# Performance work log

Hardware: AMD Instinct MI355X
Metric: run time of the kernel (lower is better)

Reference implementation:

```python
import jax, jax.numpy as jnp
import numpy as np

B, F, T, K = 16, 256, 2048, 20
TEMP = 0.5
EPS = 1e-8  # torch cosine_similarity eps


def setup_inputs() -> dict:
    key = jax.random.key(0)
    k1, k2, k3 = jax.random.split(key, 3)
    z = jax.random.normal(k1, (B, F, T), dtype=jnp.float32)
    c = jax.random.normal(k2, (B, F, T + 1), dtype=jnp.float32)
    # torch: torch.randint(0, full_len - 1, size=(B, T * K))  -> values in [0, T-2]
    negative_inds = jax.random.randint(k3, (B, T * K), 0, T - 1, dtype=jnp.int64)
    return {"z": z, "c": c, "negative_inds": negative_inds}


def reference(z, c, negative_inds):
    # ---- _generate_negatives ----
    # z: [B, F, T] -> flat rows [B*T, F]
    z_flat = jnp.transpose(z, (0, 2, 1)).reshape(-1, F)
    # per-batch offset i*T (torch adds it in-place for i in 1..B-1)
    inds = negative_inds + (jnp.arange(B, dtype=negative_inds.dtype) * T)[:, None]
    negatives = z_flat[inds.reshape(-1)].reshape(B, T, K, F)

    # ---- _calculate_similarity ----
    c_t = jnp.transpose(c[..., 1:], (0, 2, 1))[:, :, None, :]  # [B, T, 1, F] (drop start token)
    z_t = jnp.transpose(z, (0, 2, 1))[:, :, None, :]           # [B, T, 1, F]
    neg_is_pos = jnp.all(c_t == negatives, axis=-1)            # [B, T, K]
    targets = jnp.concatenate([c_t, negatives], axis=-2)       # [B, T, K+1, F]

    num = jnp.sum(z_t * targets, axis=-1)                      # [B, T, K+1]
    denom = jnp.maximum(
        jnp.linalg.norm(z_t, axis=-1) * jnp.linalg.norm(targets, axis=-1), EPS
    )
    logits = (num / denom) / TEMP                              # [B, T, K+1]

    # mask negatives that exactly equal the positive (wav2vec2-style)
    pad = jnp.zeros_like(neg_is_pos[..., :1])
    full_mask = jnp.concatenate([pad, neg_is_pos], axis=-1)    # [B, T, K+1]
    logits = jnp.where(full_mask, -jnp.inf, logits)

    return logits.reshape(-1, K + 1)                           # [B*T, K+1]
```

## Files before the change

### kernel.cpp

```cpp
#include <hip/hip_runtime.h>
#include <hip/hip_fp16.h>
#include <math.h>

#define B_ 16
#define F_ 256
#define T_ 2048
#define K_ 20
#define OUTK 21
#define NPAIR 10

typedef float v2f __attribute__((ext_vector_type(2)));

#if __has_builtin(__builtin_amdgcn_cvt_pk_f32_fp8) && __has_builtin(__builtin_amdgcn_cvt_pk_fp8_f32)
#define HW_FP8 1
#else
#define HW_FP8 0
#endif

#if !HW_FP8
__device__ __forceinline__ float dec_fp8(unsigned v) {
    unsigned s = (v >> 7) & 1, e = (v >> 3) & 15, m = v & 7;
    float r = e ? __uint_as_float(((e + 120u) << 23) | (m << 20))
                : (float)m * 0.001953125f;
    return s ? -r : r;
}
__device__ __forceinline__ unsigned enc_fp8(float x) {
    unsigned bits = __float_as_uint(x);
    unsigned s = bits >> 31;
    unsigned a = bits & 0x7fffffffu;
    float ax = __uint_as_float(a);
    unsigned r;
    if (ax < 0.015625f) {
        r = (unsigned)(int)(ax * 512.f + 0.5f);
    } else {
        int e = (int)(a >> 23) - 127;
        unsigned m = a & 0x7fffffu;
        unsigned keep = m >> 20, rest = m & 0xFFFFFu;
        keep += (rest > 0x80000u) || (rest == 0x80000u && (keep & 1));
        if (keep == 8) { keep = 0; ++e; }
        r = ((unsigned)(e + 7) << 3) | keep;
    }
    return (s << 7) | r;
}
#endif

__device__ __forceinline__ unsigned pack_fp8x4(float a0, float a1, float a2, float a3) {
#if HW_FP8
    int u = 0;
    u = __builtin_amdgcn_cvt_pk_fp8_f32(a0, a1, u, false);
    u = __builtin_amdgcn_cvt_pk_fp8_f32(a2, a3, u, true);
    return (unsigned)u;
#else
    return enc_fp8(a0) | (enc_fp8(a1) << 8) | (enc_fp8(a2) << 16) | (enc_fp8(a3) << 24);
#endif
}
template <bool HI>
__device__ __forceinline__ v2f unpk_fp8(unsigned u) {
#if HW_FP8
    return __builtin_amdgcn_cvt_pk_f32_fp8((int)u, HI);
#else
    v2f r; unsigned x = HI ? (u >> 16) : u;
    r[0] = dec_fp8(x & 0xFF); r[1] = dec_fp8((x >> 8) & 0xFF);
    return r;
#endif
}

__global__ __launch_bounds__(256) void prep_kernel(
    const float* __restrict__ z, const float* __restrict__ c,
    unsigned char* __restrict__ zf8, unsigned char* __restrict__ cf8)
{
    __shared__ float tile[256][33];
    __shared__ float ps[32][9];
    __shared__ float sc[32];
    int which = blockIdx.z;
    const float* src = which ? c : z;
    unsigned char* dst = which ? cf8 : zf8;
    int Lsrc = which ? (T_ + 1) : T_;
    int co   = which;

    int b  = blockIdx.y;
    int t0 = blockIdx.x * 32;
    const float* srcb = src + (size_t)b * F_ * Lsrc;
    int tl = threadIdx.x & 31;
    int fl = threadIdx.x >> 5;
#pragma unroll
    for (int i = 0; i < 32; ++i) {
        int f = i * 8 + fl;
        tile[f][tl] = srcb[(size_t)f * Lsrc + (t0 + tl + co)];
    }
    __syncthreads();
    {
        int col = threadIdx.x & 31, oct = threadIdx.x >> 5;
        float s = 0.f;
#pragma unroll 8
        for (int q = 0; q < 32; ++q) {
            float v = tile[oct * 32 + q][col];
            s = fmaf(v, v, s);
        }
        ps[col][oct] = s;
    }
    __syncthreads();
    if (threadIdx.x < 32) {
        float s = 0.f;
#pragma unroll
        for (int o = 0; o < 8; ++o) s += ps[threadIdx.x][o];
        float n = sqrtf(s);
        sc[threadIdx.x] = (n > 0.f) ? (1.0f / n) : 0.f;
    }
    __syncthreads();
    {
        int j = threadIdx.x & 63, r4 = threadIdx.x >> 6;
#pragma unroll
        for (int it = 0; it < 8; ++it) {
            int row = it * 4 + r4;
            float s = sc[row];
            unsigned u = pack_fp8x4(tile[2 * j][row] * s, tile[2 * j + 1][row] * s,
                                    tile[2 * j + 128][row] * s, tile[2 * j + 129][row] * s);
            ((unsigned*)(dst + ((size_t)b * T_ + t0 + row) * F_))[j] = u;
        }
    }
}

__device__ __forceinline__ float dpp_half_sum(float x) {
    x += __int_as_float(__builtin_amdgcn_mov_dpp(__float_as_int(x), 0x111, 0xF, 0xF, true));
    x += __int_as_float(__builtin_amdgcn_mov_dpp(__float_as_int(x), 0x112, 0xF, 0xF, true));
    x += __int_as_float(__builtin_amdgcn_mov_dpp(__float_as_int(x), 0x114, 0xF, 0xF, true));
    x += __int_as_float(__builtin_amdgcn_mov_dpp(__float_as_int(x), 0x118, 0xF, 0xF, true));
    x += __int_as_float(__builtin_amdgcn_mov_dpp(__float_as_int(x), 0x142, 0xF, 0xF, true));
    return x;
}

__global__ __launch_bounds__(256, 8) void sim_kernel(
    const unsigned char* __restrict__ zf8, const unsigned char* __restrict__ cf8,
    const int* __restrict__ inds, float* __restrict__ out)
{
    __shared__ float sd[128];
    int i = blockIdx.x;
    int b = (i & 7) | ((i >= 4096) ? 8 : 0);
    int wid = threadIdx.x >> 6;
    int t = (((i >> 3) & 511) << 2) + wid;
    int lane = threadIdx.x & 63;
    int hl = lane & 31;
    int hi = lane >> 5;
    int bt = __builtin_amdgcn_readfirstlane((b << 11) + t);

    const int* myinds = inds + bt * K_;
    int idxv = myinds[(lane < K_) ? lane : 0];

    uint2 zv8 = ((const uint2*)(zf8 + (size_t)bt * F_))[hl];
    uint2 cv8 = ((const uint2*)(cf8 + (size_t)bt * F_))[hl];

    const char* tbl8 = (const char*)zf8;
    unsigned zbase8  = (unsigned)(b << 11) * 256u;
    unsigned laneoff = (unsigned)hl * 8u;

    uint2 tv[NPAIR];
#pragma unroll
    for (int p = 0; p < NPAIR; ++p) {
        unsigned ilo = (unsigned)__builtin_amdgcn_readlane(idxv, 2 * p);
        unsigned ihi = (unsigned)__builtin_amdgcn_readlane(idxv, 2 * p + 1);
        unsigned off = zbase8 + (hi ? ihi : ilo) * 256u + laneoff;
        tv[p] = *(const uint2*)(tbl8 + off);
    }

    __builtin_amdgcn_sched_barrier(0);

    float zf[8];
    {
        v2f a01 = unpk_fp8<false>(zv8.x), a23 = unpk_fp8<true>(zv8.x);
        v2f a45 = unpk_fp8<false>(zv8.y), a67 = unpk_fp8<true>(zv8.y);
        zf[0] = a01[0]; zf[1] = a01[1]; zf[2] = a23[0]; zf[3] = a23[1];
        zf[4] = a45[0]; zf[5] = a45[1]; zf[6] = a67[0]; zf[7] = a67[1];
    }

    float dc;
    {
        v2f c01 = unpk_fp8<false>(cv8.x), c23 = unpk_fp8<true>(cv8.x);
        v2f c45 = unpk_fp8<false>(cv8.y), c67 = unpk_fp8<true>(cv8.y);
        float d = zf[0] * c01[0];
        d = fmaf(zf[1], c01[1], d);
        d = fmaf(zf[2], c23[0], d);
        d = fmaf(zf[3], c23[1], d);
        d = fmaf(zf[4], c45[0], d);
        d = fmaf(zf[5], c45[1], d);
        d = fmaf(zf[6], c67[0], d);
        d = fmaf(zf[7], c67[1], d);
        dc = d;
    }

    float dz[NPAIR];
#pragma unroll
    for (int p = 0; p < NPAIR; ++p) {
        v2f t01 = unpk_fp8<false>(tv[p].x), t23 = unpk_fp8<true>(tv[p].x);
        v2f t45 = unpk_fp8<false>(tv[p].y), t67 = unpk_fp8<true>(tv[p].y);
        float d = zf[0] * t01[0];
        d = fmaf(zf[1], t01[1], d);
        d = fmaf(zf[2], t23[0], d);
        d = fmaf(zf[3], t23[1], d);
        d = fmaf(zf[4], t45[0], d);
        d = fmaf(zf[5], t45[1], d);
        d = fmaf(zf[6], t67[0], d);
        d = fmaf(zf[7], t67[1], d);
        dz[p] = d;
    }

    unsigned mb = 0;
#pragma unroll
    for (int p = 0; p < NPAIR; ++p) {
        unsigned long long ball = __ballot(tv[p].x == cv8.x);
        unsigned blo = (unsigned)ball, bhi = (unsigned)(ball >> 32);
        if (blo == 0xFFFFFFFFu || bhi == 0xFFFFFFFFu) {
            bool full = (tv[p].x == cv8.x) && (tv[p].y == cv8.y);
            unsigned long long b2 = __ballot(full);
            if ((unsigned)b2 == 0xFFFFFFFFu)          mb |= 1u << (1 + 2 * p);
            if ((unsigned)(b2 >> 32) == 0xFFFFFFFFu)  mb |= 1u << (2 + 2 * p);
        }
    }

    dc = dpp_half_sum(dc);
#pragma unroll
    for (int p = 0; p < NPAIR; ++p) dz[p] = dpp_half_sum(dz[p]);

    if (hl == 31) {
        if (hi == 0) sd[wid * 32] = dc;
#pragma unroll
        for (int p = 0; p < NPAIR; ++p) sd[wid * 32 + 1 + 2 * p + hi] = dz[p];
    }

    if (lane < OUTK) {
        float v = sd[wid * 32 + lane] * 2.0f;
        if ((mb >> lane) & 1u) v = -INFINITY;
        out[(size_t)bt * OUTK + lane] = v;
    }
}

extern "C" void kernel_launch(void* const* d_in, const int* in_sizes, int n_in,
                              void* d_out, int out_size, void* d_ws, size_t ws_size,
                              hipStream_t stream)
{
    const float* z    = (const float*)d_in[0];
    const float* c    = (const float*)d_in[1];
    const int*   inds = (const int*)d_in[2];
    float* out = (float*)d_out;

    char* ws = (char*)d_ws;
    size_t f8_bytes = (size_t)B_ * T_ * F_;
    unsigned char* zf8 = (unsigned char*)ws;
    unsigned char* cf8 = (unsigned char*)(ws + f8_bytes);

    dim3 tb(256), tg(T_ / 32, B_, 2);
    prep_kernel<<<tg, tb, 0, stream>>>(z, c, zf8, cf8);
    sim_kernel<<<dim3(B_ * T_ / 4), dim3(256), 0, stream>>>(zf8, cf8, inds, out);
}
```

Baseline: 42.52 us.

## Restructure prep kernel to column-per-thread reads with swizzled fp8 LDS staging

The prep kernel now gives each thread one time column and half the features, and each block covers 128 timesteps instead of 32. Each thread reads its column twice from global memory: once to accumulate the squared norm, then again to scale and pack to fp8. The packed words go into an XOR-swizzled LDS tile, which is written out as coalesced rows. The fp32 LDS transpose tile goes away and global reads become wider contiguous spans per row. The cost is a second global pass that relies on cache hits, a changed feature-packing order (consistent across z, c and negatives), and four times fewer blocks.

Measured after the change: 50.09 us. 1.18x slower.

```diff
diff --git a/kernel.cpp b/kernel.cpp
--- a/kernel.cpp
+++ b/kernel.cpp
@@ -8,6 +8,7 @@
 #define K_ 20
 #define OUTK 21
 #define NPAIR 10
+#define TT 128
 
 typedef float v2f __attribute__((ext_vector_type(2)));
 
@@ -69,9 +70,9 @@
     const float* __restrict__ z, const float* __restrict__ c,
     unsigned char* __restrict__ zf8, unsigned char* __restrict__ cf8)
 {
-    __shared__ float tile[256][33];
-    __shared__ float ps[32][9];
-    __shared__ float sc[32];
+    __shared__ unsigned otile[TT][64];
+    __shared__ float ps[TT][2];
+    __shared__ float sc[TT];
     int which = blockIdx.z;
     const float* src = which ? c : z;
     unsigned char* dst = which ? cf8 : zf8;
@@ -79,45 +80,45 @@
     int co   = which;
 
     int b  = blockIdx.y;
-    int t0 = blockIdx.x * 32;
-    const float* srcb = src + (size_t)b * F_ * Lsrc;
-    int tl = threadIdx.x & 31;
-    int fl = threadIdx.x >> 5;
-#pragma unroll
-    for (int i = 0; i < 32; ++i) {
-        int f = i * 8 + fl;
-        tile[f][tl] = srcb[(size_t)f * Lsrc + (t0 + tl + co)];
-    }
+    int t0 = blockIdx.x * TT;
+    int tl = threadIdx.x & (TT - 1);
+    int h  = threadIdx.x >> 7;
+    const float* base = src + (size_t)b * F_ * Lsrc + ((size_t)h * 128) * Lsrc
+                      + (t0 + tl + co);
+
+    float s = 0.f;
+#pragma unroll 16
+    for (int i = 0; i < 128; ++i) {
+        float v = base[(size_t)i * Lsrc];
+        s = fmaf(v, v, s);
+    }
+    ps[tl][h] = s;
     __syncthreads();
-    {
-        int col = threadIdx.x & 31, oct = threadIdx.x >> 5;
-        float s = 0.f;
-#pragma unroll 8
-        for (int q = 0; q < 32; ++q) {
-            float v = tile[oct * 32 + q][col];
-            s = fmaf(v, v, s);
-        }
-        ps[col][oct] = s;
+    if (threadIdx.x < TT) {
+        float n = sqrtf(ps[threadIdx.x][0] + ps[threadIdx.x][1]);
+        sc[threadIdx.x] = (n > 0.f) ? (1.0f / n) : 0.f;
     }
     __syncthreads();
-    if (threadIdx.x < 32) {
-        float s = 0.f;
-#pragma unroll
-        for (int o = 0; o < 8; ++o) s += ps[threadIdx.x][o];
-        float n = sqrtf(s);
-        sc[threadIdx.x] = (n > 0.f) ? (1.0f / n) : 0.f;
+    float scale = sc[tl];
+
+#pragma unroll 4
+    for (int j = 0; j < 32; ++j) {
+        float a0 = base[(size_t)(4 * j + 0) * Lsrc] * scale;
+        float a1 = base[(size_t)(4 * j + 1) * Lsrc] * scale;
+        float a2 = base[(size_t)(4 * j + 2) * Lsrc] * scale;
+        float a3 = base[(size_t)(4 * j + 3) * Lsrc] * scale;
+        unsigned u = pack_fp8x4(a0, a1, a2, a3);
+        int d = h * 32 + j;
+        otile[tl][d ^ (tl & 31)] = u;
     }
     __syncthreads();
-    {
-        int j = threadIdx.x & 63, r4 = threadIdx.x >> 6;
-#pragma unroll
-        for (int it = 0; it < 8; ++it) {
-            int row = it * 4 + r4;
-            float s = sc[row];
-            unsigned u = pack_fp8x4(tile[2 * j][row] * s, tile[2 * j + 1][row] * s,
-                                    tile[2 * j + 128][row] * s, tile[2 * j + 129][row] * s);
-            ((unsigned*)(dst + ((size_t)b * T_ + t0 + row) * F_))[j] = u;
-        }
+
+    int wid = threadIdx.x >> 6, lane = threadIdx.x & 63;
+#pragma unroll
+    for (int r4 = 0; r4 < TT / 4; ++r4) {
+        int r = r4 * 4 + wid;
+        unsigned u = otile[r][lane ^ (r & 31)];
+        ((unsigned*)(dst + ((size_t)b * T_ + t0 + r) * F_))[lane] = u;
     }
 }
 
@@ -248,7 +249,7 @@
     unsigned char* zf8 = (unsigned char*)ws;
     unsigned char* cf8 = (unsigned char*)(ws + f8_bytes);
 
-    dim3 tb(256), tg(T_ / 32, B_, 2);
+    dim3 tb(256), tg(T_ / TT, B_, 2);
     prep_kernel<<<tg, tb, 0, stream>>>(z, c, zf8, cf8);
     sim_kernel<<<dim3(B_ * T_ / 4), dim3(256), 0, stream>>>(zf8, cf8, inds, out);
 }
```

## Replace LDS transpose in prep kernel with register-resident per-thread feature rows

Applied to the files above, without the earlier changes.

The prep kernel no longer stages a 256x32 tile in shared memory. Each thread now loads 64 features of one time step into registers, computes the partial norm there, and packs and stores 64 contiguous fp8 bytes with 128-bit writes. Blocks cover 64 time steps, and shared memory holds only the small norm reduction, so the tile writes, tile reads and one barrier are gone. The fp8 byte order within a row changes to consecutive features. That is safe because the sim kernel reads z, c and the negatives in the same layout and only uses order-independent dot products and equality checks. The costs are higher register pressure, fewer blocks, and stores strided by 256 bytes across lanes.

Result: no change. 41.90 us (-1.4%).

```diff
diff --git a/kernel.cpp b/kernel.cpp
--- a/kernel.cpp
+++ b/kernel.cpp
@@ -69,9 +69,8 @@
     const float* __restrict__ z, const float* __restrict__ c,
     unsigned char* __restrict__ zf8, unsigned char* __restrict__ cf8)
 {
-    __shared__ float tile[256][33];
-    __shared__ float ps[32][9];
-    __shared__ float sc[32];
+    __shared__ float ps[64][5];
+    __shared__ float sc[64];
     int which = blockIdx.z;
     const float* src = which ? c : z;
     unsigned char* dst = which ? cf8 : zf8;
@@ -79,45 +78,46 @@
     int co   = which;
 
     int b  = blockIdx.y;
-    int t0 = blockIdx.x * 32;
-    const float* srcb = src + (size_t)b * F_ * Lsrc;
-    int tl = threadIdx.x & 31;
-    int fl = threadIdx.x >> 5;
-#pragma unroll
-    for (int i = 0; i < 32; ++i) {
-        int f = i * 8 + fl;
-        tile[f][tl] = srcb[(size_t)f * Lsrc + (t0 + tl + co)];
-    }
+    int t0 = blockIdx.x * 64;
+    int t  = threadIdx.x & 63;
+    int q  = threadIdx.x >> 6;
+
+    const float* base = src + ((size_t)b * F_ + (size_t)q * 64) * Lsrc + (t0 + t + co);
+
+    float vals[64];
+    float s0 = 0.f, s1 = 0.f, s2 = 0.f, s3 = 0.f;
+#pragma unroll
+    for (int i = 0; i < 64; i += 4) {
+        vals[i]     = base[(size_t)(i)     * Lsrc];
+        vals[i + 1] = base[(size_t)(i + 1) * Lsrc];
+        vals[i + 2] = base[(size_t)(i + 2) * Lsrc];
+        vals[i + 3] = base[(size_t)(i + 3) * Lsrc];
+        s0 = fmaf(vals[i],     vals[i],     s0);
+        s1 = fmaf(vals[i + 1], vals[i + 1], s1);
+        s2 = fmaf(vals[i + 2], vals[i + 2], s2);
+        s3 = fmaf(vals[i + 3], vals[i + 3], s3);
+    }
+    ps[t][q] = (s0 + s1) + (s2 + s3);
     __syncthreads();
-    {
-        int col = threadIdx.x & 31, oct = threadIdx.x >> 5;
-        float s = 0.f;
-#pragma unroll 8
-        for (int q = 0; q < 32; ++q) {
-            float v = tile[oct * 32 + q][col];
-            s = fmaf(v, v, s);
-        }
-        ps[col][oct] = s;
-    }
-    __syncthreads();
-    if (threadIdx.x < 32) {
-        float s = 0.f;
-#pragma unroll
-        for (int o = 0; o < 8; ++o) s += ps[threadIdx.x][o];
+    if (threadIdx.x < 64) {
+        float s = (ps[threadIdx.x][0] + ps[threadIdx.x][1])
+                + (ps[threadIdx.x][2] + ps[threadIdx.x][3]);
         float n = sqrtf(s);
         sc[threadIdx.x] = (n > 0.f) ? (1.0f / n) : 0.f;
     }
     __syncthreads();
-    {
-        int j = threadIdx.x & 63, r4 = threadIdx.x >> 6;
-#pragma unroll
-        for (int it = 0; it < 8; ++it) {
-            int row = it * 4 + r4;
-            float s = sc[row];
-            unsigned u = pack_fp8x4(tile[2 * j][row] * s, tile[2 * j + 1][row] * s,
-                                    tile[2 * j + 128][row] * s, tile[2 * j + 129][row] * s);
-            ((unsigned*)(dst + ((size_t)b * T_ + t0 + row) * F_))[j] = u;
-        }
+    float scale = sc[t];
+
+    unsigned u[16];
+#pragma unroll
+    for (int j = 0; j < 16; ++j)
+        u[j] = pack_fp8x4(vals[4 * j] * scale, vals[4 * j + 1] * scale,
+                          vals[4 * j + 2] * scale, vals[4 * j + 3] * scale);
+    uint4* orow = (uint4*)(dst + ((size_t)b * T_ + t0 + t) * F_ + (size_t)q * 64);
+#pragma unroll
+    for (int j4 = 0; j4 < 4; ++j4) {
+        uint4 vv = {u[4 * j4], u[4 * j4 + 1], u[4 * j4 + 2], u[4 * j4 + 3]};
+        orow[j4] = vv;
     }
 }
 
@@ -248,7 +248,7 @@
     unsigned char* zf8 = (unsigned char*)ws;
     unsigned char* cf8 = (unsigned char*)(ws + f8_bytes);
 
-    dim3 tb(256), tg(T_ / 32, B_, 2);
+    dim3 tb(256), tg(T_ / 64, B_, 2);
     prep_kernel<<<tg, tb, 0, stream>>>(z, c, zf8, cf8);
     sim_kernel<<<dim3(B_ * T_ / 4), dim3(256), 0, stream>>>(zf8, cf8, inds, out);
 }
```
